# Kernel optimization log

Hardware: AMD Instinct MI355X
Metric: run time of the kernel (lower is better)

The kernel has to match this reference:

```python
import jax, jax.numpy as jnp
import numpy as np
import math

D_MODEL = 256
H = 8
D_K = D_MODEL // H
POS_OFFSET = 20
GRID = 7  # module hard-codes key_padding_mask.view(bs, 7, 7)


def _sine_pos_table(num_pos_feats=D_MODEL // 2, temperature=10000, rng=(-20, 20)):
    # faithful port of position_embedding_sine with normalize=True
    scale = 2 * math.pi
    emb = np.arange(rng[0], rng[1] + 1, dtype=np.float32)
    emb = emb / (emb[-1] + 1e-6) * scale  # normalize by last element (=20)
    dim_t = np.arange(num_pos_feats, dtype=np.float32)
    dim_t = temperature ** (2.0 * np.floor(dim_t / 2.0) / num_pos_feats)
    pos = emb[:, None] / dim_t  # [41, 128]
    pos = np.stack((np.sin(pos[:, 0::2]), np.cos(pos[:, 1::2])), axis=-1).reshape(pos.shape[0], -1)
    return jnp.asarray(pos, dtype=jnp.float32)  # [41, 128]


def setup_inputs() -> dict:
    key = jax.random.key(0)
    ks = jax.random.split(key, 8)
    L, B, D = 49, 2048, D_MODEL
    query = jax.random.normal(ks[0], (L, B, D), dtype=jnp.float32)
    key_t = jax.random.normal(ks[1], (L, B, D), dtype=jnp.float32)
    value = jax.random.normal(ks[2], (L, B, D), dtype=jnp.float32)
    key_padding_mask = jnp.zeros((B, L), dtype=bool)  # no padding
    # parameters (xavier-ish init)
    lim = math.sqrt(6.0 / (3 * D + D))
    in_proj_weight = jax.random.uniform(ks[3], (3 * D, D), minval=-lim, maxval=lim, dtype=jnp.float32)
    in_proj_bias = jnp.zeros((3 * D,), dtype=jnp.float32)
    out_w = jax.random.uniform(ks[4], (D, D), minval=-1.0 / math.sqrt(D), maxval=1.0 / math.sqrt(D), dtype=jnp.float32)
    out_b = jnp.zeros((D,), dtype=jnp.float32)
    pos_x = _sine_pos_table()  # [41, 128]
    pos_y = _sine_pos_table()  # [41, 128]
    return {"query": query, "key": key_t, "value": value,
            "key_padding_mask": key_padding_mask,
            "in_proj_weight": in_proj_weight, "in_proj_bias": in_proj_bias,
            "out_w": out_w, "out_b": out_b, "pos_x": pos_x, "pos_y": pos_y}


def reference(query, key, value, key_padding_mask, in_proj_weight, in_proj_bias, out_w, out_b, pos_x, pos_y):
    L, B, D = query.shape
    S = key.shape[0]
    scaling = float(D_K) ** -0.5
    w_q, w_k, w_v = in_proj_weight[:D], in_proj_weight[D:2 * D], in_proj_weight[2 * D:]
    b_q, b_k, b_v = in_proj_bias[:D], in_proj_bias[D:2 * D], in_proj_bias[2 * D:]
    q = (query @ w_q.T + b_q) * scaling          # [L, B, D]
    k = key @ w_k.T + b_k                        # [S, B, D]
    v = value @ w_v.T + b_v                      # [S, B, D]
    # [B, H, L, d_k] etc.
    q4 = q.reshape(L, B, H, D_K).transpose(1, 2, 0, 3)
    k4 = k.reshape(S, B, H, D_K).transpose(1, 2, 0, 3)
    v4 = v.reshape(S, B, H, D_K).transpose(1, 2, 0, 3)
    attn = jnp.einsum('bhld,bhsd->bhls', q4, k4)  # [B, H, L, S]
    # relative position indices from cumsum over the 7x7 grid
    img_mask = (~key_padding_mask).reshape(B, GRID, GRID)
    yy = jnp.cumsum(img_mask.astype(jnp.float32), axis=1).reshape(B, -1)
    xx = jnp.cumsum(img_mask.astype(jnp.float32), axis=2).reshape(B, -1)
    idx_yy = (yy[:, :, None] - yy[:, None, :] + POS_OFFSET).astype(jnp.int32)  # [B, HW, HW]
    idx_xx = (xx[:, :, None] - xx[:, None, :] + POS_OFFSET).astype(jnp.int32)
    # project positional tables through the key weights (faithful slicing)
    k_posy = jnp.einsum('pf,df->pd', pos_y, w_k[:, :D // 2])  # [41, D]
    k_posx = jnp.einsum('pf,df->pd', pos_x, w_k[:, D // 2:])  # [41, D]
    P = k_posy.shape[0]
    k_posy = k_posy.reshape(P, H, D_K)
    k_posx = k_posx.reshape(P, H, D_K)
    posy = jnp.einsum('bhld,phd->bhlp', q4, k_posy)  # [B, H, HW, 41]
    posx = jnp.einsum('bhld,phd->bhlp', q4, k_posx)
    gy = jnp.take_along_axis(posy, jnp.broadcast_to(idx_yy[:, None], posy.shape[:3] + (S,)), axis=-1)
    gx = jnp.take_along_axis(posx, jnp.broadcast_to(idx_xx[:, None], posx.shape[:3] + (S,)), axis=-1)
    attn = attn + gy + gx
    attn = jnp.where(key_padding_mask[:, None, None, :], -jnp.inf, attn)
    attn = jax.nn.softmax(attn, axis=-1)  # dropout skipped (eval mode)
    out = jnp.einsum('bhls,bhsd->bhld', attn, v4)        # [B, H, L, d_k]
    out = out.transpose(2, 0, 1, 3).reshape(L, B, D)     # [L, B, D]
    out = out @ out_w.T + out_b
    return out
```

## Files before the change

kernel.cpp:

```cpp
#include <hip/hip_runtime.h>
#include <hip/hip_bf16.h>

#define L_Q 49
#define D_MODEL 256
#define NHEAD 8
#define DK 32
#define PP 41
#define POS_OFF 20

typedef __attribute__((ext_vector_type(8))) __bf16 bf16x8;
typedef __attribute__((ext_vector_type(4))) float f32x4;
typedef __attribute__((ext_vector_type(8))) unsigned short u16x8;

__device__ __forceinline__ float bf2f(unsigned short u) {
    return __uint_as_float(((unsigned)u) << 16);
}
__device__ __forceinline__ unsigned short f2bf(float f) {
    unsigned u = __float_as_uint(f);
    return (unsigned short)((u + 0x7FFF + ((u >> 16) & 1)) >> 16);
}

__global__ __launch_bounds__(256)
void convert_w(const float* __restrict__ W, const float* __restrict__ out_w,
               float scaling,
               unsigned short* __restrict__ wbf, unsigned short* __restrict__ owbf) {
    int i = blockIdx.x * 256 + threadIdx.x;
    if (i < 49152) {
        int row = i >> 6;
        float sc = (row < 256) ? scaling : 1.0f;
        float4 v = reinterpret_cast<const float4*>(W)[i];
        ushort4 o = { f2bf(v.x * sc), f2bf(v.y * sc), f2bf(v.z * sc), f2bf(v.w * sc) };
        reinterpret_cast<ushort4*>(wbf)[i] = o;
    } else {
        float4 v = reinterpret_cast<const float4*>(out_w)[i - 49152];
        ushort4 o = { f2bf(v.x), f2bf(v.y), f2bf(v.z), f2bf(v.w) };
        reinterpret_cast<ushort4*>(owbf)[i - 49152] = o;
    }
}

__global__ __launch_bounds__(256)
void prep_kpos(const float* __restrict__ pos_y, const float* __restrict__ pos_x,
               const float* __restrict__ W, unsigned short* __restrict__ kpb) {
    int p = blockIdx.x;
    int which = blockIdx.y;
    __shared__ float pr[128];
    int d = threadIdx.x;
    if (d < 128) pr[d] = which ? pos_x[p * 128 + d] : pos_y[p * 128 + d];
    __syncthreads();
    const float* Wk = W + 256 * 256;
    int fOff = which ? 128 : 0;
    float acc = 0.f;
    #pragma unroll 8
    for (int f = 0; f < 128; ++f)
        acc += pr[f] * Wk[(size_t)d * 256 + fOff + f];
    kpb[((size_t)which * PP + p) * 256 + d] = f2bf(acc);
}

__global__ __launch_bounds__(512)
void proj_mfma(const float* __restrict__ Xq, const float* __restrict__ Xk,
               const float* __restrict__ Xv,
               const unsigned short* __restrict__ Wb,
               const float* __restrict__ bias, float scaling,
               unsigned short* __restrict__ outq, unsigned short* __restrict__ outk,
               unsigned short* __restrict__ outv) {
    __shared__ unsigned char Sz[65536];
    __shared__ float Lb[256];
    int which = blockIdx.y;
    const float* X = (which == 0) ? Xq : ((which == 1) ? Xk : Xv);
    unsigned short* out = (which == 0) ? outq : ((which == 1) ? outk : outv);
    const char* wsrc = (const char*)(Wb + (size_t)which * 65536);

    int tid = threadIdx.x, wid = tid >> 6, lane = tid & 63;
    int rgrp = lane & 15, kgrp = lane >> 4;
    int wm = wid & 1, wn = wid >> 1;
    size_t tile0 = (size_t)blockIdx.x * 128;
    const char* xsrc = (const char*)X;

    auto stage = [&](int kk, int buf) {
        #pragma unroll
        for (int it = 0; it < 2; ++it) {
            int c = wid + it * 8;
            {
                int arow = c * 8 + (lane >> 3);
                unsigned off = (unsigned)(lane & 7) * 16;
                unsigned gs = (unsigned)(kk * 128) + (off ^ (((unsigned)arow & 7) << 4));
                __builtin_amdgcn_global_load_lds(
                    xsrc + (tile0 + arow) * 1024 + gs,
                    (char*)Sz + buf * 16384 + c * 1024 + lane * 16, 16, 0, 0);
            }
            {
                int ncol = c * 16 + (lane >> 2);
                unsigned off = (unsigned)(lane & 3) * 16;
                unsigned gs = (unsigned)ncol * 512 + (unsigned)(kk * 64)
                            + (off ^ (((unsigned)ncol & 3) << 4));
                __builtin_amdgcn_global_load_lds(
                    wsrc + gs,
                    (char*)Sz + 32768 + buf * 16384 + c * 1024 + lane * 16, 16, 0, 0);
            }
        }
    };

    stage(0, 0);
    if (tid < 256) Lb[tid] = bias[which * 256 + tid] * ((which == 0) ? scaling : 1.0f);
    __syncthreads();

    f32x4 acc[4][4];
    #pragma unroll
    for (int m = 0; m < 4; ++m)
        #pragma unroll
        for (int n = 0; n < 4; ++n) acc[m][n] = (f32x4){0.f, 0.f, 0.f, 0.f};

    int buf = 0;
    for (int kk = 0; kk < 8; ++kk) {
        if (kk < 7) stage(kk + 1, buf ^ 1);

        const char* Az = (const char*)Sz + buf * 16384;
        const char* Bz = (const char*)Sz + 32768 + buf * 16384;

        bf16x8 bf[4];
        #pragma unroll
        for (int nt = 0; nt < 4; ++nt) {
            int ncol = wn * 64 + nt * 16 + rgrp;
            unsigned ad = (unsigned)ncol * 64
                        + (((unsigned)kgrp * 16) ^ (((unsigned)ncol & 3) << 4));
            bf[nt] = *reinterpret_cast<const bf16x8*>(Bz + ad);
        }
        #pragma unroll
        for (int mf = 0; mf < 4; ++mf) {
            int arow = wm * 64 + mf * 16 + rgrp;
            unsigned s = ((unsigned)arow & 7) << 4;
            unsigned a1 = (unsigned)arow * 128 + (((unsigned)kgrp * 32) ^ s);
            unsigned a2 = (unsigned)arow * 128 + (((unsigned)kgrp * 32 + 16) ^ s);
            f32x4 q0 = *reinterpret_cast<const f32x4*>(Az + a1);
            f32x4 q1 = *reinterpret_cast<const f32x4*>(Az + a2);
            bf16x8 af;
            af[0] = (__bf16)q0[0]; af[1] = (__bf16)q0[1];
            af[2] = (__bf16)q0[2]; af[3] = (__bf16)q0[3];
            af[4] = (__bf16)q1[0]; af[5] = (__bf16)q1[1];
            af[6] = (__bf16)q1[2]; af[7] = (__bf16)q1[3];
            #pragma unroll
            for (int nt = 0; nt < 4; ++nt)
                acc[mf][nt] = __builtin_amdgcn_mfma_f32_16x16x32_bf16(bf[nt], af, acc[mf][nt], 0, 0, 0);
        }
        __syncthreads();
        buf ^= 1;
    }

    #pragma unroll
    for (int mf = 0; mf < 4; ++mf) {
        size_t xrow = tile0 + wm * 64 + mf * 16 + rgrp;
        #pragma unroll
        for (int nt = 0; nt < 4; ++nt) {
            int col = wn * 64 + nt * 16 + kgrp * 4;
            float4 bv = *reinterpret_cast<const float4*>(&Lb[col]);
            ushort4 pk;
            pk.x = f2bf(acc[mf][nt][0] + bv.x);
            pk.y = f2bf(acc[mf][nt][1] + bv.y);
            pk.z = f2bf(acc[mf][nt][2] + bv.z);
            pk.w = f2bf(acc[mf][nt][3] + bv.w);
            *reinterpret_cast<ushort4*>(&out[xrow * 256 + col]) = pk;
        }
    }
}

__global__ __launch_bounds__(512)
void out_mfma(const unsigned short* __restrict__ Xb, const unsigned short* __restrict__ Wb,
              const float* __restrict__ bias, float* __restrict__ out) {
    __shared__ unsigned char Sz[49152];
    __shared__ float Lb[256];
    int tid = threadIdx.x, wid = tid >> 6, lane = tid & 63;
    int rgrp = lane & 15, kgrp = lane >> 4;
    int wm = wid & 1, wn = wid >> 1;
    size_t tile0 = (size_t)blockIdx.x * 128;
    const char* xsrc = (const char*)Xb;
    const char* wsrc = (const char*)Wb;

    auto stage = [&](int kk, int buf) {
        {
            int arow = wid * 16 + (lane >> 2);
            unsigned off = (unsigned)(lane & 3) * 16;
            unsigned gs = (unsigned)(kk * 64) + (off ^ (((unsigned)arow & 3) << 4));
            __builtin_amdgcn_global_load_lds(
                xsrc + (tile0 + arow) * 512 + gs,
                (char*)Sz + buf * 8192 + wid * 1024 + lane * 16, 16, 0, 0);
        }
        #pragma unroll
        for (int it = 0; it < 2; ++it) {
            int c = wid + it * 8;
            int ncol = c * 16 + (lane >> 2);
            unsigned off = (unsigned)(lane & 3) * 16;
            unsigned gs = (unsigned)ncol * 512 + (unsigned)(kk * 64)
                        + (off ^ (((unsigned)ncol & 3) << 4));
            __builtin_amdgcn_global_load_lds(
                wsrc + gs,
                (char*)Sz + 16384 + buf * 16384 + c * 1024 + lane * 16, 16, 0, 0);
        }
    };

    stage(0, 0);
    if (tid < 256) Lb[tid] = bias[tid];
    __syncthreads();

    f32x4 acc[4][4];
    #pragma unroll
    for (int m = 0; m < 4; ++m)
        #pragma unroll
        for (int n = 0; n < 4; ++n) acc[m][n] = (f32x4){0.f, 0.f, 0.f, 0.f};

    int buf = 0;
    for (int kk = 0; kk < 8; ++kk) {
        if (kk < 7) stage(kk + 1, buf ^ 1);

        const char* Az = (const char*)Sz + buf * 8192;
        const char* Bz = (const char*)Sz + 16384 + buf * 16384;

        bf16x8 bf[4];
        #pragma unroll
        for (int nt = 0; nt < 4; ++nt) {
            int ncol = wn * 64 + nt * 16 + rgrp;
            unsigned ad = (unsigned)ncol * 64
                        + (((unsigned)kgrp * 16) ^ (((unsigned)ncol & 3) << 4));
            bf[nt] = *reinterpret_cast<const bf16x8*>(Bz + ad);
        }
        #pragma unroll
        for (int mf = 0; mf < 4; ++mf) {
            int arow = wm * 64 + mf * 16 + rgrp;
            unsigned ad = (unsigned)arow * 64
                        + (((unsigned)kgrp * 16) ^ (((unsigned)arow & 3) << 4));
            bf16x8 af = *reinterpret_cast<const bf16x8*>(Az + ad);
            #pragma unroll
            for (int nt = 0; nt < 4; ++nt)
                acc[mf][nt] = __builtin_amdgcn_mfma_f32_16x16x32_bf16(bf[nt], af, acc[mf][nt], 0, 0, 0);
        }
        __syncthreads();
        buf ^= 1;
    }

    #pragma unroll
    for (int mf = 0; mf < 4; ++mf) {
        size_t xrow = tile0 + wm * 64 + mf * 16 + rgrp;
        #pragma unroll
        for (int nt = 0; nt < 4; ++nt) {
            int col = wn * 64 + nt * 16 + kgrp * 4;
            float4 bv = *reinterpret_cast<const float4*>(&Lb[col]);
            float4 o;
            o.x = acc[mf][nt][0] + bv.x;
            o.y = acc[mf][nt][1] + bv.y;
            o.z = acc[mf][nt][2] + bv.z;
            o.w = acc[mf][nt][3] + bv.w;
            *reinterpret_cast<float4*>(&out[xrow * 256 + col]) = o;
        }
    }
}

__global__ __launch_bounds__(256)
void attn_mfma(const unsigned short* __restrict__ qbuf,
               const unsigned short* __restrict__ kbuf,
               const unsigned short* __restrict__ vbuf,
               const unsigned short* __restrict__ kpb,
               const unsigned char* __restrict__ mask,
               unsigned short* __restrict__ ctx,
               int B) {
    __shared__ unsigned short Kp[96][40];
    __shared__ unsigned short Pt[64][72];
    __shared__ unsigned short Vt[32][72];
    __shared__ unsigned short postab[49][40];
    __shared__ int yy[L_Q], xx[L_Q];
    __shared__ unsigned char mb[52];

    int b = blockIdx.x, h = blockIdx.y;
    int tid = threadIdx.x, wid = tid >> 6, lane = tid & 63;
    int rgrp = lane & 15, kgrp = lane >> 4;
    size_t lstride = (size_t)B * D_MODEL;
    size_t base = (size_t)b * D_MODEL + (size_t)h * DK;

    if (tid < L_Q) mb[tid] = mask[(size_t)b * L_Q + tid];
    if (tid < 196) {
        int l = tid >> 2, c = tid & 3;
        u16x8 vv = *reinterpret_cast<const u16x8*>(vbuf + (size_t)l * lstride + base + c * 8);
        #pragma unroll
        for (int j = 0; j < 8; ++j) Vt[c * 8 + j][l] = vv[j];
    }
    for (int e = tid; e < 512; e += 256) {
        int d = e >> 4, s2 = 48 + (e & 15);
        if (s2 > 48) Vt[d][s2] = 0;
    }
    for (int t = tid; t < 384; t += 256) {
        int r = t >> 2, kc = t & 3;
        const unsigned short* src;
        if (r < 64) {
            int kr = min(r, 48);
            src = kbuf + (size_t)kr * lstride + base + kc * 8;
        } else if (r < 80) {
            int p = r - 64 + 13;
            src = kpb + (size_t)p * D_MODEL + h * DK + kc * 8;
        } else {
            int p = r - 80 + 13;
            src = kpb + (size_t)(PP + p) * D_MODEL + h * DK + kc * 8;
        }
        *reinterpret_cast<u16x8*>(&Kp[r][kc * 8]) = *reinterpret_cast<const u16x8*>(src);
    }
    __syncthreads();
    if (tid < L_Q) {
        int r = tid / 7, c = tid % 7;
        int sy = 0, sx = 0;
        for (int rr = 0; rr <= r; ++rr) sy += (mb[rr * 7 + c] == 0);
        for (int cc = 0; cc <= c; ++cc) sx += (mb[r * 7 + cc] == 0);
        yy[tid] = sy; xx[tid] = sx;
    }
    __syncthreads();

    int qrow = min(16 * wid + rgrp, 48);
    bf16x8 qfrag = *reinterpret_cast<const bf16x8*>(qbuf + (size_t)qrow * lstride + base + kgrp * 8);
    f32x4 acc[6];
    #pragma unroll
    for (int t = 0; t < 6; ++t) {
        bf16x8 bfrag = *reinterpret_cast<const bf16x8*>(&Kp[t * 16 + rgrp][kgrp * 8]);
        acc[t] = __builtin_amdgcn_mfma_f32_16x16x32_bf16(qfrag, bfrag,
                    (f32x4){0.f, 0.f, 0.f, 0.f}, 0, 0, 0);
    }

    #pragma unroll
    for (int i = 0; i < 4; ++i) {
        int l = 16 * wid + kgrp * 4 + i;
        if (l <= 48) {
            postab[l][rgrp]      = f2bf(acc[4][i]);
            postab[l][20 + rgrp] = f2bf(acc[5][i]);
        }
    }
    asm volatile("s_waitcnt lgkmcnt(0)" ::: "memory");

    #pragma unroll
    for (int i = 0; i < 4; ++i) {
        int l = 16 * wid + kgrp * 4 + i;
        int lc = min(l, 48);
        int yyl = yy[lc], xxl = xx[lc];
        float v[4];
        #pragma unroll
        for (int ct = 0; ct < 4; ++ct) {
            int s = ct * 16 + rgrp;
            int sc = min(s, 48);
            int iy = yyl - yy[sc] + (POS_OFF - 13);
            int ix = xxl - xx[sc] + (POS_OFF - 13);
            float val = acc[ct][i] + bf2f(postab[lc][iy]) + bf2f(postab[lc][20 + ix]);
            v[ct] = (s >= L_Q || mb[sc]) ? -1e30f : val;
        }
        float m = fmaxf(fmaxf(v[0], v[1]), fmaxf(v[2], v[3]));
        m = fmaxf(m, __shfl_xor(m, 1));
        m = fmaxf(m, __shfl_xor(m, 2));
        m = fmaxf(m, __shfl_xor(m, 4));
        m = fmaxf(m, __shfl_xor(m, 8));
        float ssum = 0.f, ex[4];
        #pragma unroll
        for (int ct = 0; ct < 4; ++ct) { ex[ct] = __expf(v[ct] - m); ssum += ex[ct]; }
        ssum += __shfl_xor(ssum, 1);
        ssum += __shfl_xor(ssum, 2);
        ssum += __shfl_xor(ssum, 4);
        ssum += __shfl_xor(ssum, 8);
        float is = 1.f / ssum;
        #pragma unroll
        for (int ct = 0; ct < 4; ++ct)
            Pt[l & 63][ct * 16 + rgrp] = f2bf(ex[ct] * is);
    }
    asm volatile("s_waitcnt lgkmcnt(0)" ::: "memory");

    f32x4 oacc[2];
    oacc[0] = (f32x4){0.f, 0.f, 0.f, 0.f};
    oacc[1] = (f32x4){0.f, 0.f, 0.f, 0.f};
    #pragma unroll
    for (int kc = 0; kc < 2; ++kc) {
        bf16x8 pa = *reinterpret_cast<const bf16x8*>(&Pt[16 * wid + rgrp][kc * 32 + kgrp * 8]);
        #pragma unroll
        for (int dt = 0; dt < 2; ++dt) {
            bf16x8 vb = *reinterpret_cast<const bf16x8*>(&Vt[dt * 16 + rgrp][kc * 32 + kgrp * 8]);
            oacc[dt] = __builtin_amdgcn_mfma_f32_16x16x32_bf16(pa, vb, oacc[dt], 0, 0, 0);
        }
    }
    #pragma unroll
    for (int dt = 0; dt < 2; ++dt)
        #pragma unroll
        for (int i = 0; i < 4; ++i) {
            int l = 16 * wid + kgrp * 4 + i;
            if (l <= 48)
                ctx[(size_t)l * lstride + base + dt * 16 + rgrp] = f2bf(oacc[dt][i]);
        }
}

extern "C" void kernel_launch(void* const* d_in, const int* in_sizes, int n_in,
                              void* d_out, int out_size, void* d_ws, size_t ws_size,
                              hipStream_t stream) {
    const float* query = (const float*)d_in[0];
    const float* key   = (const float*)d_in[1];
    const float* value = (const float*)d_in[2];
    const unsigned char* maskp = (const unsigned char*)d_in[3];
    const float* W     = (const float*)d_in[4];
    const float* bias  = (const float*)d_in[5];
    const float* out_w = (const float*)d_in[6];
    const float* out_b = (const float*)d_in[7];
    const float* pos_x = (const float*)d_in[8];
    const float* pos_y = (const float*)d_in[9];
    float* out = (float*)d_out;

    int B = in_sizes[0] / (L_Q * D_MODEL);
    int M = L_Q * B;

    size_t nqkv = (size_t)M * D_MODEL;
    unsigned short* qb = (unsigned short*)d_ws;
    unsigned short* kb = qb + nqkv;
    unsigned short* vb = kb + nqkv;
    unsigned short* kpb = vb + nqkv;
    unsigned short* wbf = kpb + 2 * PP * D_MODEL;
    unsigned short* owbf = wbf + 768 * 256;

    const float scaling = 0.17677669529663687f;

    convert_w<<<256, 256, 0, stream>>>(W, out_w, scaling, wbf, owbf);
    prep_kpos<<<dim3(PP, 2), 256, 0, stream>>>(pos_y, pos_x, W, kpb);

    int tiles = M / 128;
    proj_mfma<<<dim3(tiles, 3), 512, 0, stream>>>(query, key, value, wbf, bias, scaling,
                                                  qb, kb, vb);

    attn_mfma<<<dim3(B, NHEAD), 256, 0, stream>>>(qb, kb, vb, kpb, maskp, qb, B);

    out_mfma<<<tiles, 512, 0, stream>>>(qb, owbf, out_b, out);
}
```

Before: 274.4 us.

## Deepen projection GEMM prefetch to two stages with explicit vmcnt waits

The projection GEMM now issues two tile loads up front and, in each iteration, waits only until the current buffer's async global-to-LDS loads have landed. It then reads every A and B fragment into registers, barriers, and starts the load for tile kk+2 into the just-freed buffer before running the MFMAs. This is meant to hide global load latency behind the MFMA work instead of serializing on a full syncthreads each step. The hand-written waitcnt counts depend on how many load instructions stage() issues per thread, so a miscount could cause a data race. The bias write to Lb now has no barrier of its own and relies on the first in-loop barrier being reached before the epilogue reads it.

```diff
diff --git a/kernel.cpp b/kernel.cpp
--- a/kernel.cpp
+++ b/kernel.cpp
@@ -100,9 +100,9 @@
         }
     };
 
+    if (tid < 256) Lb[tid] = bias[which * 256 + tid] * ((which == 0) ? scaling : 1.0f);
     stage(0, 0);
-    if (tid < 256) Lb[tid] = bias[which * 256 + tid] * ((which == 0) ? scaling : 1.0f);
-    __syncthreads();
+    stage(1, 1);
 
     f32x4 acc[4][4];
     #pragma unroll
@@ -110,14 +110,17 @@
         #pragma unroll
         for (int n = 0; n < 4; ++n) acc[m][n] = (f32x4){0.f, 0.f, 0.f, 0.f};
 
-    int buf = 0;
+    #pragma unroll
     for (int kk = 0; kk < 8; ++kk) {
-        if (kk < 7) stage(kk + 1, buf ^ 1);
+        int buf = kk & 1;
+        if (kk < 7) asm volatile("s_waitcnt vmcnt(4)" ::: "memory");
+        else        asm volatile("s_waitcnt vmcnt(0)" ::: "memory");
+        __builtin_amdgcn_s_barrier();
 
         const char* Az = (const char*)Sz + buf * 16384;
         const char* Bz = (const char*)Sz + 32768 + buf * 16384;
 
-        bf16x8 bf[4];
+        bf16x8 bf[4], af[4];
         #pragma unroll
         for (int nt = 0; nt < 4; ++nt) {
             int ncol = wn * 64 + nt * 16 + rgrp;
@@ -129,21 +132,23 @@
         for (int mf = 0; mf < 4; ++mf) {
             int arow = wm * 64 + mf * 16 + rgrp;
             unsigned s = ((unsigned)arow & 7) << 4;
-            unsigned a1 = (unsigned)arow * 128 + (((unsigned)kgrp * 32) ^ s);
-            unsigned a2 = (unsigned)arow * 128 + (((unsigned)kgrp * 32 + 16) ^ s);
-            f32x4 q0 = *reinterpret_cast<const f32x4*>(Az + a1);
-            f32x4 q1 = *reinterpret_cast<const f32x4*>(Az + a2);
-            bf16x8 af;
-            af[0] = (__bf16)q0[0]; af[1] = (__bf16)q0[1];
-            af[2] = (__bf16)q0[2]; af[3] = (__bf16)q0[3];
-            af[4] = (__bf16)q1[0]; af[5] = (__bf16)q1[1];
-            af[6] = (__bf16)q1[2]; af[7] = (__bf16)q1[3];
+            f32x4 q0 = *reinterpret_cast<const f32x4*>(Az + (unsigned)arow * 128 + (((unsigned)kgrp * 32) ^ s));
+            f32x4 q1 = *reinterpret_cast<const f32x4*>(Az + (unsigned)arow * 128 + (((unsigned)kgrp * 32 + 16) ^ s));
+            af[mf][0] = (__bf16)q0[0]; af[mf][1] = (__bf16)q0[1];
+            af[mf][2] = (__bf16)q0[2]; af[mf][3] = (__bf16)q0[3];
+            af[mf][4] = (__bf16)q1[0]; af[mf][5] = (__bf16)q1[1];
+            af[mf][6] = (__bf16)q1[2]; af[mf][7] = (__bf16)q1[3];
+        }
+        asm volatile("s_waitcnt lgkmcnt(0)" ::: "memory");
+        __builtin_amdgcn_sched_barrier(0);
+        __builtin_amdgcn_s_barrier();
+        if (kk < 6) stage(kk + 2, buf);
+
+        #pragma unroll
+        for (int mf = 0; mf < 4; ++mf)
             #pragma unroll
             for (int nt = 0; nt < 4; ++nt)
-                acc[mf][nt] = __builtin_amdgcn_mfma_f32_16x16x32_bf16(bf[nt], af, acc[mf][nt], 0, 0, 0);
-        }
-        __syncthreads();
-        buf ^= 1;
+                acc[mf][nt] = __builtin_amdgcn_mfma_f32_16x16x32_bf16(bf[nt], af[mf], acc[mf][nt], 0, 0, 0);
     }
 
     #pragma unroll
```

After: 286.4 us. 4.3% more time.

## Process two heads per attention block and merge prep kernels into one launch

Applied to the files above, without the earlier changes.

The attention kernel now handles two heads per block with 512 threads, so each batch index has half as many blocks. Loads of K, V and the positional tables are widened to cover 64 contiguous columns per row, which is meant to improve coalescing and cut per-block setup such as the mask and yy/xx computation. The weight-conversion and positional-key projection kernels are merged into one launch to save launch overhead. The cost is double the shared memory per block and larger blocks, which may lower occupancy.

```diff
diff --git a/kernel.cpp b/kernel.cpp
--- a/kernel.cpp
+++ b/kernel.cpp
@@ -21,39 +21,40 @@
 }
 
 __global__ __launch_bounds__(256)
-void convert_w(const float* __restrict__ W, const float* __restrict__ out_w,
-               float scaling,
-               unsigned short* __restrict__ wbf, unsigned short* __restrict__ owbf) {
-    int i = blockIdx.x * 256 + threadIdx.x;
-    if (i < 49152) {
-        int row = i >> 6;
-        float sc = (row < 256) ? scaling : 1.0f;
-        float4 v = reinterpret_cast<const float4*>(W)[i];
-        ushort4 o = { f2bf(v.x * sc), f2bf(v.y * sc), f2bf(v.z * sc), f2bf(v.w * sc) };
-        reinterpret_cast<ushort4*>(wbf)[i] = o;
+void prep_all(const float* __restrict__ W, const float* __restrict__ out_w,
+              const float* __restrict__ pos_y, const float* __restrict__ pos_x,
+              float scaling,
+              unsigned short* __restrict__ wbf, unsigned short* __restrict__ owbf,
+              unsigned short* __restrict__ kpb) {
+    int bx = blockIdx.x;
+    if (bx < 256) {
+        int i = bx * 256 + threadIdx.x;
+        if (i < 49152) {
+            int row = i >> 6;
+            float sc = (row < 256) ? scaling : 1.0f;
+            float4 v = reinterpret_cast<const float4*>(W)[i];
+            ushort4 o = { f2bf(v.x * sc), f2bf(v.y * sc), f2bf(v.z * sc), f2bf(v.w * sc) };
+            reinterpret_cast<ushort4*>(wbf)[i] = o;
+        } else {
+            float4 v = reinterpret_cast<const float4*>(out_w)[i - 49152];
+            ushort4 o = { f2bf(v.x), f2bf(v.y), f2bf(v.z), f2bf(v.w) };
+            reinterpret_cast<ushort4*>(owbf)[i - 49152] = o;
+        }
     } else {
-        float4 v = reinterpret_cast<const float4*>(out_w)[i - 49152];
-        ushort4 o = { f2bf(v.x), f2bf(v.y), f2bf(v.z), f2bf(v.w) };
-        reinterpret_cast<ushort4*>(owbf)[i - 49152] = o;
-    }
-}
-
-__global__ __launch_bounds__(256)
-void prep_kpos(const float* __restrict__ pos_y, const float* __restrict__ pos_x,
-               const float* __restrict__ W, unsigned short* __restrict__ kpb) {
-    int p = blockIdx.x;
-    int which = blockIdx.y;
-    __shared__ float pr[128];
-    int d = threadIdx.x;
-    if (d < 128) pr[d] = which ? pos_x[p * 128 + d] : pos_y[p * 128 + d];
-    __syncthreads();
-    const float* Wk = W + 256 * 256;
-    int fOff = which ? 128 : 0;
-    float acc = 0.f;
-    #pragma unroll 8
-    for (int f = 0; f < 128; ++f)
-        acc += pr[f] * Wk[(size_t)d * 256 + fOff + f];
-    kpb[((size_t)which * PP + p) * 256 + d] = f2bf(acc);
+        int q = bx - 256;
+        int which = q / PP, p = q % PP;
+        __shared__ float pr[128];
+        int d = threadIdx.x;
+        if (d < 128) pr[d] = which ? pos_x[p * 128 + d] : pos_y[p * 128 + d];
+        __syncthreads();
+        const float* Wk = W + 256 * 256;
+        int fOff = which ? 128 : 0;
+        float acc = 0.f;
+        #pragma unroll 8
+        for (int f = 0; f < 128; ++f)
+            acc += pr[f] * Wk[(size_t)d * 256 + fOff + f];
+        kpb[((size_t)which * PP + p) * 256 + d] = f2bf(acc);
+    }
 }
 
 __global__ __launch_bounds__(512)
@@ -253,7 +254,7 @@
     }
 }
 
-__global__ __launch_bounds__(256)
+__global__ __launch_bounds__(512)
 void attn_mfma(const unsigned short* __restrict__ qbuf,
                const unsigned short* __restrict__ kbuf,
                const unsigned short* __restrict__ vbuf,
@@ -261,44 +262,48 @@
                const unsigned char* __restrict__ mask,
                unsigned short* __restrict__ ctx,
                int B) {
-    __shared__ unsigned short Kp[96][40];
-    __shared__ unsigned short Pt[64][72];
-    __shared__ unsigned short Vt[32][72];
-    __shared__ unsigned short postab[49][40];
+    __shared__ unsigned short Kp[2][96][40];
+    __shared__ unsigned short Pt[2][64][72];
+    __shared__ unsigned short Vt[2][32][72];
+    __shared__ unsigned short postab[2][49][40];
     __shared__ int yy[L_Q], xx[L_Q];
     __shared__ unsigned char mb[52];
 
-    int b = blockIdx.x, h = blockIdx.y;
+    int b = blockIdx.x, hg = blockIdx.y;
     int tid = threadIdx.x, wid = tid >> 6, lane = tid & 63;
+    int w4 = wid & 3, lh = wid >> 2;
     int rgrp = lane & 15, kgrp = lane >> 4;
     size_t lstride = (size_t)B * D_MODEL;
-    size_t base = (size_t)b * D_MODEL + (size_t)h * DK;
+    size_t base = (size_t)b * D_MODEL + (size_t)hg * 64;
 
     if (tid < L_Q) mb[tid] = mask[(size_t)b * L_Q + tid];
-    if (tid < 196) {
-        int l = tid >> 2, c = tid & 3;
-        u16x8 vv = *reinterpret_cast<const u16x8*>(vbuf + (size_t)l * lstride + base + c * 8);
-        #pragma unroll
-        for (int j = 0; j < 8; ++j) Vt[c * 8 + j][l] = vv[j];
-    }
-    for (int e = tid; e < 512; e += 256) {
-        int d = e >> 4, s2 = 48 + (e & 15);
-        if (s2 > 48) Vt[d][s2] = 0;
-    }
-    for (int t = tid; t < 384; t += 256) {
-        int r = t >> 2, kc = t & 3;
+    if (tid < 392) {
+        int l = tid >> 3, c = tid & 7;
+        int vlh = c >> 2, cc = c & 3;
+        u16x8 vv = *reinterpret_cast<const u16x8*>(
+            vbuf + (size_t)l * lstride + base + vlh * 32 + cc * 8);
+        #pragma unroll
+        for (int j = 0; j < 8; ++j) Vt[vlh][cc * 8 + j][l] = vv[j];
+    }
+    for (int e = tid; e < 1024; e += 512) {
+        int zlh = e >> 9, r = e & 511;
+        int d = r >> 4, s2 = 48 + (r & 15);
+        if (s2 > 48) Vt[zlh][d][s2] = 0;
+    }
+    {
+        int r = tid >> 3, c = tid & 7, klh = c >> 2, kc = c & 3;
+        int kr = min(r, 48);
+        const unsigned short* src = kbuf + (size_t)kr * lstride + base + klh * 32 + kc * 8;
+        *reinterpret_cast<u16x8*>(&Kp[klh][r][kc * 8]) = *reinterpret_cast<const u16x8*>(src);
+    }
+    if (tid < 256) {
+        int r2 = tid >> 3, c = tid & 7, klh = c >> 2, kc = c & 3;
         const unsigned short* src;
-        if (r < 64) {
-            int kr = min(r, 48);
-            src = kbuf + (size_t)kr * lstride + base + kc * 8;
-        } else if (r < 80) {
-            int p = r - 64 + 13;
-            src = kpb + (size_t)p * D_MODEL + h * DK + kc * 8;
-        } else {
-            int p = r - 80 + 13;
-            src = kpb + (size_t)(PP + p) * D_MODEL + h * DK + kc * 8;
-        }
-        *reinterpret_cast<u16x8*>(&Kp[r][kc * 8]) = *reinterpret_cast<const u16x8*>(src);
+        if (r2 < 16)
+            src = kpb + (size_t)(r2 + 13) * 256 + hg * 64 + klh * 32 + kc * 8;
+        else
+            src = kpb + (size_t)(PP + r2 - 16 + 13) * 256 + hg * 64 + klh * 32 + kc * 8;
+        *reinterpret_cast<u16x8*>(&Kp[klh][64 + r2][kc * 8]) = *reinterpret_cast<const u16x8*>(src);
     }
     __syncthreads();
     if (tid < L_Q) {
@@ -310,29 +315,30 @@
     }
     __syncthreads();
 
-    int qrow = min(16 * wid + rgrp, 48);
-    bf16x8 qfrag = *reinterpret_cast<const bf16x8*>(qbuf + (size_t)qrow * lstride + base + kgrp * 8);
+    int qrow = min(16 * w4 + rgrp, 48);
+    bf16x8 qfrag = *reinterpret_cast<const bf16x8*>(
+        qbuf + (size_t)qrow * lstride + base + lh * 32 + kgrp * 8);
     f32x4 acc[6];
     #pragma unroll
     for (int t = 0; t < 6; ++t) {
-        bf16x8 bfrag = *reinterpret_cast<const bf16x8*>(&Kp[t * 16 + rgrp][kgrp * 8]);
+        bf16x8 bfrag = *reinterpret_cast<const bf16x8*>(&Kp[lh][t * 16 + rgrp][kgrp * 8]);
         acc[t] = __builtin_amdgcn_mfma_f32_16x16x32_bf16(qfrag, bfrag,
                     (f32x4){0.f, 0.f, 0.f, 0.f}, 0, 0, 0);
     }
 
     #pragma unroll
     for (int i = 0; i < 4; ++i) {
-        int l = 16 * wid + kgrp * 4 + i;
+        int l = 16 * w4 + kgrp * 4 + i;
         if (l <= 48) {
-            postab[l][rgrp]      = f2bf(acc[4][i]);
-            postab[l][20 + rgrp] = f2bf(acc[5][i]);
+            postab[lh][l][rgrp]      = f2bf(acc[4][i]);
+            postab[lh][l][20 + rgrp] = f2bf(acc[5][i]);
         }
     }
     asm volatile("s_waitcnt lgkmcnt(0)" ::: "memory");
 
     #pragma unroll
     for (int i = 0; i < 4; ++i) {
-        int l = 16 * wid + kgrp * 4 + i;
+        int l = 16 * w4 + kgrp * 4 + i;
         int lc = min(l, 48);
         int yyl = yy[lc], xxl = xx[lc];
         float v[4];
@@ -342,7 +348,7 @@
             int sc = min(s, 48);
             int iy = yyl - yy[sc] + (POS_OFF - 13);
             int ix = xxl - xx[sc] + (POS_OFF - 13);
-            float val = acc[ct][i] + bf2f(postab[lc][iy]) + bf2f(postab[lc][20 + ix]);
+            float val = acc[ct][i] + bf2f(postab[lh][lc][iy]) + bf2f(postab[lh][lc][20 + ix]);
             v[ct] = (s >= L_Q || mb[sc]) ? -1e30f : val;
         }
         float m = fmaxf(fmaxf(v[0], v[1]), fmaxf(v[2], v[3]));
@@ -360,7 +366,7 @@
         float is = 1.f / ssum;
         #pragma unroll
         for (int ct = 0; ct < 4; ++ct)
-            Pt[l & 63][ct * 16 + rgrp] = f2bf(ex[ct] * is);
+            Pt[lh][l & 63][ct * 16 + rgrp] = f2bf(ex[ct] * is);
     }
     asm volatile("s_waitcnt lgkmcnt(0)" ::: "memory");
 
@@ -369,10 +375,10 @@
     oacc[1] = (f32x4){0.f, 0.f, 0.f, 0.f};
     #pragma unroll
     for (int kc = 0; kc < 2; ++kc) {
-        bf16x8 pa = *reinterpret_cast<const bf16x8*>(&Pt[16 * wid + rgrp][kc * 32 + kgrp * 8]);
+        bf16x8 pa = *reinterpret_cast<const bf16x8*>(&Pt[lh][16 * w4 + rgrp][kc * 32 + kgrp * 8]);
         #pragma unroll
         for (int dt = 0; dt < 2; ++dt) {
-            bf16x8 vb = *reinterpret_cast<const bf16x8*>(&Vt[dt * 16 + rgrp][kc * 32 + kgrp * 8]);
+            bf16x8 vb = *reinterpret_cast<const bf16x8*>(&Vt[lh][dt * 16 + rgrp][kc * 32 + kgrp * 8]);
             oacc[dt] = __builtin_amdgcn_mfma_f32_16x16x32_bf16(pa, vb, oacc[dt], 0, 0, 0);
         }
     }
@@ -380,9 +386,9 @@
     for (int dt = 0; dt < 2; ++dt)
         #pragma unroll
         for (int i = 0; i < 4; ++i) {
-            int l = 16 * wid + kgrp * 4 + i;
+            int l = 16 * w4 + kgrp * 4 + i;
             if (l <= 48)
-                ctx[(size_t)l * lstride + base + dt * 16 + rgrp] = f2bf(oacc[dt][i]);
+                ctx[(size_t)l * lstride + base + lh * 32 + dt * 16 + rgrp] = f2bf(oacc[dt][i]);
         }
 }
 
@@ -414,14 +420,14 @@
 
     const float scaling = 0.17677669529663687f;
 
-    convert_w<<<256, 256, 0, stream>>>(W, out_w, scaling, wbf, owbf);
-    prep_kpos<<<dim3(PP, 2), 256, 0, stream>>>(pos_y, pos_x, W, kpb);
+    prep_all<<<256 + 2 * PP, 256, 0, stream>>>(W, out_w, pos_y, pos_x, scaling,
+                                               wbf, owbf, kpb);
 
     int tiles = M / 128;
     proj_mfma<<<dim3(tiles, 3), 512, 0, stream>>>(query, key, value, wbf, bias, scaling,
                                                   qb, kb, vb);
 
-    attn_mfma<<<dim3(B, NHEAD), 256, 0, stream>>>(qb, kb, vb, kpb, maskp, qb, B);
+    attn_mfma<<<dim3(B, NHEAD / 2), 512, 0, stream>>>(qb, kb, vb, kpb, maskp, qb, B);
 
     out_mfma<<<tiles, 512, 0, stream>>>(qb, owbf, out_b, out);
 }
```

Result: no change. 270.9 us (-1.3%).
